# Performance work log

Measured on AMD Instinct MI355X. Metric: run time of the kernel, lower is better.

## Reference

```python
import jax, jax.numpy as jnp
import numpy as np

N_NODES = 50000
N_EDGES = 800000
IN_DIM = 256
OUT_DIM = 64
NEG_SLOPE = 0.01  # torch F.leaky_relu default


def setup_inputs() -> dict:
    key = jax.random.key(0)
    k1, k2, k3, k4, k5 = jax.random.split(key, 5)
    return {
        "h": jax.random.normal(k1, (N_NODES, IN_DIM), dtype=jnp.float32),
        "src": jax.random.randint(k2, (N_EDGES,), 0, N_NODES, dtype=jnp.int32),
        "dst": jax.random.randint(k3, (N_EDGES,), 0, N_NODES, dtype=jnp.int32),
        "W_fc": jax.random.normal(k4, (IN_DIM, OUT_DIM), dtype=jnp.float32) / np.sqrt(IN_DIM),
        "a_vec": jax.random.normal(k5, (2 * OUT_DIM,), dtype=jnp.float32) / np.sqrt(2 * OUT_DIM),
    }


def reference(h, src, dst, W_fc, a_vec):
    n = h.shape[0]
    d = W_fc.shape[1]
    # z = fc(h)
    z = h @ W_fc  # [N, out_dim]
    # edge attention: attn_fc(cat[z_src, z_dst]) == z_src@a[:d] + z_dst@a[d:]
    s_src = z @ a_vec[:d]  # [N]
    s_dst = z @ a_vec[d:]  # [N]
    e = jax.nn.leaky_relu(s_src[src] + s_dst[dst], negative_slope=NEG_SLOPE)  # [E]
    # segment softmax over incoming edges of each dst node (stable)
    e_max = jax.ops.segment_max(e, dst, num_segments=n)  # -inf for isolated nodes (unused)
    e_exp = jnp.exp(e - e_max[dst])
    denom = jax.ops.segment_sum(e_exp, dst, num_segments=n)
    alpha = e_exp / denom[dst]  # [E]
    # weighted scatter-sum of source features
    out = jax.ops.segment_sum(alpha[:, None] * z[src], dst, num_segments=n)  # [N, out_dim]
    return out
```

## Files before the change

kernel.cpp:

```cpp
#include <hip/hip_runtime.h>

#define IN_DIM 256
#define OUT_DIM 64
#define NEG_SLOPE 0.01f
#define SCAN_CHUNK 2048
#define HBS 280

typedef short short8 __attribute__((ext_vector_type(8)));
typedef float f32x4 __attribute__((ext_vector_type(4)));
typedef unsigned short u16x4 __attribute__((ext_vector_type(4)));
typedef unsigned short u16x8 __attribute__((ext_vector_type(8)));

__device__ __forceinline__ unsigned short f2b(float f) {
    unsigned u = __float_as_uint(f);
    return (unsigned short)((u + 0x7FFFu + ((u >> 16) & 1u)) >> 16);
}
__device__ __forceinline__ float b2f(unsigned short b) {
    return __uint_as_float(((unsigned)b) << 16);
}

__global__ __launch_bounds__(256) void w_conv(const float* __restrict__ W,
                                              unsigned short* __restrict__ Wt) {
    int g = blockIdx.x * 256 + threadIdx.x;
    int k = g >> 6, c = g & 63;
    Wt[c * IN_DIM + k] = f2b(W[k * OUT_DIM + c]);
}

__global__ __launch_bounds__(256) void gemm_mfma(const float* __restrict__ h,
                                                 const unsigned short* __restrict__ Wt,
                                                 const float* __restrict__ a,
                                                 unsigned short* __restrict__ zb,
                                                 float* __restrict__ s_src,
                                                 float* __restrict__ s_dst, int n) {
    __shared__ unsigned short hb[64 * HBS];
    __shared__ unsigned short wb[64 * HBS];
    __shared__ float sp1[2][64];
    __shared__ float sp2[2][64];
    const int tid = threadIdx.x;
    const int lane = tid & 63;
    const int w = tid >> 6;
    const int row0 = blockIdx.x * 64;

    {
        int c = tid >> 2, seg = tid & 3;
        #pragma unroll
        for (int i = 0; i < 8; ++i) {
            u16x8 v = *(const u16x8*)&Wt[c * IN_DIM + seg * 64 + i * 8];
            *(u16x8*)&wb[c * HBS + seg * 64 + i * 8] = v;
        }
    }
    {
        int r = tid >> 2, seg = tid & 3;
        int grow = row0 + r;
        #pragma unroll
        for (int i = 0; i < 16; ++i) {
            float4 hv = make_float4(0.f, 0.f, 0.f, 0.f);
            if (grow < n)
                hv = *(const float4*)&h[(size_t)grow * IN_DIM + seg * 64 + i * 4];
            u16x4 p;
            p[0] = f2b(hv.x); p[1] = f2b(hv.y); p[2] = f2b(hv.z); p[3] = f2b(hv.w);
            *(u16x4*)&hb[r * HBS + seg * 64 + i * 4] = p;
        }
    }
    __syncthreads();

    const int rw = (w & 1) * 32;
    const int cw = (w >> 1) * 32;
    const int l16 = lane & 15;
    const int q = lane >> 4;

    f32x4 acc[2][2] = {};
    #pragma unroll
    for (int ks = 0; ks < 8; ++ks) {
        short8 af[2], bf[2];
        #pragma unroll
        for (int i = 0; i < 2; ++i)
            af[i] = *(const short8*)&hb[(rw + i * 16 + l16) * HBS + ks * 32 + q * 8];
        #pragma unroll
        for (int j = 0; j < 2; ++j)
            bf[j] = *(const short8*)&wb[(cw + j * 16 + l16) * HBS + ks * 32 + q * 8];
        #pragma unroll
        for (int i = 0; i < 2; ++i)
            #pragma unroll
            for (int j = 0; j < 2; ++j)
                acc[i][j] = __builtin_amdgcn_mfma_f32_16x16x32_bf16(af[i], bf[j], acc[i][j], 0, 0, 0);
    }

    #pragma unroll
    for (int i = 0; i < 2; ++i) {
        #pragma unroll
        for (int reg = 0; reg < 4; ++reg) {
            int row_local = rw + i * 16 + q * 4 + reg;
            int grow = row0 + row_local;
            float p1 = 0.f, p2 = 0.f;
            #pragma unroll
            for (int j = 0; j < 2; ++j) {
                int col = cw + j * 16 + l16;
                float zv = acc[i][j][reg];
                if (grow < n) zb[(size_t)grow * OUT_DIM + col] = f2b(zv);
                p1 = fmaf(zv, a[col], p1);
                p2 = fmaf(zv, a[OUT_DIM + col], p2);
            }
            #pragma unroll
            for (int o = 1; o < 16; o <<= 1) {
                p1 += __shfl_xor(p1, o);
                p2 += __shfl_xor(p2, o);
            }
            if (l16 == 0) {
                sp1[w >> 1][row_local] = p1;
                sp2[w >> 1][row_local] = p2;
            }
        }
    }
    __syncthreads();
    if (tid < 64) {
        int grow = row0 + tid;
        if (grow < n) {
            s_src[grow] = sp1[0][tid] + sp1[1][tid];
            s_dst[grow] = sp2[0][tid] + sp2[1][tid];
        }
    }
}

__global__ __launch_bounds__(256) void count_deg(const int* __restrict__ dst,
                                                 int* __restrict__ deg,
                                                 int* __restrict__ rank, int E) {
    int i = blockIdx.x * 256 + threadIdx.x;
    if (i >= E) return;
    rank[i] = atomicAdd(&deg[dst[i]], 1);
}

__global__ __launch_bounds__(256) void block_sums(const int* __restrict__ deg,
                                                  int* __restrict__ bsum, int n) {
    __shared__ int red[256];
    const int tid = threadIdx.x;
    int base = blockIdx.x * SCAN_CHUNK + tid * 8;
    int s = 0;
    #pragma unroll
    for (int j = 0; j < 8; ++j)
        if (base + j < n) s += deg[base + j];
    red[tid] = s;
    __syncthreads();
    #pragma unroll
    for (int d = 128; d; d >>= 1) {
        if (tid < d) red[tid] += red[tid + d];
        __syncthreads();
    }
    if (tid == 0) bsum[blockIdx.x] = red[0];
}

__global__ __launch_bounds__(256) void scan_bsums(const int* __restrict__ bsum,
                                                  int* __restrict__ ebase,
                                                  int* __restrict__ off, int nb, int n) {
    __shared__ int ts[256];
    const int tid = threadIdx.x;
    int v = (tid < nb) ? bsum[tid] : 0;
    ts[tid] = v;
    __syncthreads();
    #pragma unroll
    for (int d = 1; d < 256; d <<= 1) {
        int add = (tid >= d) ? ts[tid - d] : 0;
        __syncthreads();
        ts[tid] += add;
        __syncthreads();
    }
    if (tid < nb) ebase[tid] = ts[tid] - v;
    if (tid == 255) off[n] = ts[255];
}

__global__ __launch_bounds__(256) void scan_local(const int* __restrict__ deg,
                                                  const int* __restrict__ ebase,
                                                  int* __restrict__ off, int n) {
    __shared__ int ts[256];
    const int tid = threadIdx.x;
    int base = blockIdx.x * SCAN_CHUNK + tid * 8;
    int v[8];
    int s = 0;
    #pragma unroll
    for (int j = 0; j < 8; ++j) {
        v[j] = (base + j < n) ? deg[base + j] : 0;
        s += v[j];
    }
    ts[tid] = s;
    __syncthreads();
    #pragma unroll
    for (int d = 1; d < 256; d <<= 1) {
        int add = (tid >= d) ? ts[tid - d] : 0;
        __syncthreads();
        ts[tid] += add;
        __syncthreads();
    }
    int run = ebase[blockIdx.x] + ts[tid] - s;
    #pragma unroll
    for (int j = 0; j < 8; ++j) {
        if (base + j < n) off[base + j] = run;
        run += v[j];
    }
}

__global__ __launch_bounds__(256) void scatter_csr(const int* __restrict__ src,
                                                   const int* __restrict__ dst,
                                                   const float* __restrict__ s_src,
                                                   const float* __restrict__ s_dst,
                                                   const int* __restrict__ off,
                                                   const int* __restrict__ rank,
                                                   int2* __restrict__ csr, int E) {
    int i = blockIdx.x * 256 + threadIdx.x;
    if (i >= E) return;
    int s = src[i], t = dst[i];
    float x = s_src[s] + s_dst[t];
    x = x > 0.f ? x : NEG_SLOPE * x;
    float w = __expf(x);
    int pos = off[t] + rank[i];
    csr[pos] = make_int2(s, __float_as_int(w));
}

__global__ __launch_bounds__(256) void aggregate(const int* __restrict__ off,
                                                 const int2* __restrict__ csr,
                                                 const unsigned short* __restrict__ zb,
                                                 float* __restrict__ out, int n) {
    int node = blockIdx.x * 4 + (threadIdx.x >> 6);
    int lane = threadIdx.x & 63;
    if (node >= n) return;
    int beg = off[node];
    int end = off[node + 1];

    float acc = 0.f;
    float s = 0.f;
    int j = beg;
    for (; j + 3 < end; j += 4) {
        int2 e0 = csr[j];
        int2 e1 = csr[j + 1];
        int2 e2 = csr[j + 2];
        int2 e3 = csr[j + 3];
        float w0 = __int_as_float(e0.y);
        float w1 = __int_as_float(e1.y);
        float w2 = __int_as_float(e2.y);
        float w3 = __int_as_float(e3.y);
        float z0 = b2f(zb[(size_t)e0.x * OUT_DIM + lane]);
        float z1 = b2f(zb[(size_t)e1.x * OUT_DIM + lane]);
        float z2 = b2f(zb[(size_t)e2.x * OUT_DIM + lane]);
        float z3 = b2f(zb[(size_t)e3.x * OUT_DIM + lane]);
        acc = fmaf(w0, z0, acc);
        acc = fmaf(w1, z1, acc);
        acc = fmaf(w2, z2, acc);
        acc = fmaf(w3, z3, acc);
        s += (w0 + w1) + (w2 + w3);
    }
    for (; j < end; ++j) {
        int2 e0 = csr[j];
        float w0 = __int_as_float(e0.y);
        acc = fmaf(w0, b2f(zb[(size_t)e0.x * OUT_DIM + lane]), acc);
        s += w0;
    }
    float inv = (end > beg) ? 1.0f / s : 0.f;
    out[(size_t)node * OUT_DIM + lane] = acc * inv;
}

extern "C" void kernel_launch(void* const* d_in, const int* in_sizes, int n_in,
                              void* d_out, int out_size, void* d_ws, size_t ws_size,
                              hipStream_t stream) {
    const float* h   = (const float*)d_in[0];
    const int*   src = (const int*)d_in[1];
    const int*   dst = (const int*)d_in[2];
    const float* W   = (const float*)d_in[3];
    const float* a   = (const float*)d_in[4];
    float* out = (float*)d_out;

    const int n = in_sizes[0] / IN_DIM;
    const int E = in_sizes[1];
    const int nb = (n + SCAN_CHUNK - 1) / SCAN_CHUNK;

    char* ws = (char*)d_ws;
    size_t off_b = 0;
    auto alloc = [&](size_t bytes) -> void* {
        void* p = ws + off_b;
        off_b += (bytes + 255) & ~(size_t)255;
        return p;
    };
    unsigned short* zb   = (unsigned short*)alloc((size_t)n * OUT_DIM * sizeof(unsigned short));
    unsigned short* Wt   = (unsigned short*)alloc((size_t)IN_DIM * OUT_DIM * sizeof(unsigned short));
    float*          s_src= (float*)alloc((size_t)n * sizeof(float));
    float*          s_dst= (float*)alloc((size_t)n * sizeof(float));
    int*            deg  = (int*)alloc((size_t)n * sizeof(int));
    int*            offs = (int*)alloc((size_t)(n + 1) * sizeof(int));
    int*            rank = (int*)alloc((size_t)E * sizeof(int));
    int*            bsum = (int*)alloc(256 * sizeof(int));
    int*            ebase= (int*)alloc(256 * sizeof(int));
    int2*           csr  = (int2*)alloc((size_t)E * sizeof(int2));

    hipMemsetAsync(deg, 0, (size_t)n * sizeof(int), stream);

    w_conv<<<64, 256, 0, stream>>>(W, Wt);
    gemm_mfma<<<(n + 63) / 64, 256, 0, stream>>>(h, Wt, a, zb, s_src, s_dst, n);
    count_deg<<<(E + 255) / 256, 256, 0, stream>>>(dst, deg, rank, E);
    block_sums<<<nb, 256, 0, stream>>>(deg, bsum, n);
    scan_bsums<<<1, 256, 0, stream>>>(bsum, ebase, offs, nb, n);
    scan_local<<<nb, 256, 0, stream>>>(deg, ebase, offs, n);
    scatter_csr<<<(E + 255) / 256, 256, 0, stream>>>(src, dst, s_src, s_dst, offs,
                                                     rank, csr, E);
    aggregate<<<(n + 3) / 4, 256, 0, stream>>>(offs, csr, zb, out, n);
}
```

Measured before the change: 208.6 us.

## Fuse W conversion into GEMM, merge scan passes, vectorize aggregation

Removes the separate W transpose/convert kernel by having each GEMM block load fp32 W and write bf16 transposed into shared memory. Merges the block-sum and top-level scan kernels using a last-block ticket counter. Reworks aggregation so each wavefront processes four edges concurrently with 4-wide bf16 loads, then reduces across quarter-waves with shuffles. The aim is fewer launches and more memory parallelism, at the cost of redundant W conversion in every GEMM block and strided LDS writes.

```diff
diff --git a/kernel.cpp b/kernel.cpp
--- a/kernel.cpp
+++ b/kernel.cpp
@@ -9,7 +9,6 @@
 typedef short short8 __attribute__((ext_vector_type(8)));
 typedef float f32x4 __attribute__((ext_vector_type(4)));
 typedef unsigned short u16x4 __attribute__((ext_vector_type(4)));
-typedef unsigned short u16x8 __attribute__((ext_vector_type(8)));
 
 __device__ __forceinline__ unsigned short f2b(float f) {
     unsigned u = __float_as_uint(f);
@@ -19,15 +18,8 @@
     return __uint_as_float(((unsigned)b) << 16);
 }
 
-__global__ __launch_bounds__(256) void w_conv(const float* __restrict__ W,
-                                              unsigned short* __restrict__ Wt) {
-    int g = blockIdx.x * 256 + threadIdx.x;
-    int k = g >> 6, c = g & 63;
-    Wt[c * IN_DIM + k] = f2b(W[k * OUT_DIM + c]);
-}
-
 __global__ __launch_bounds__(256) void gemm_mfma(const float* __restrict__ h,
-                                                 const unsigned short* __restrict__ Wt,
+                                                 const float* __restrict__ W,
                                                  const float* __restrict__ a,
                                                  unsigned short* __restrict__ zb,
                                                  float* __restrict__ s_src,
@@ -42,11 +34,16 @@
     const int row0 = blockIdx.x * 64;
 
     {
-        int c = tid >> 2, seg = tid & 3;
-        #pragma unroll
-        for (int i = 0; i < 8; ++i) {
-            u16x8 v = *(const u16x8*)&Wt[c * IN_DIM + seg * 64 + i * 8];
-            *(u16x8*)&wb[c * HBS + seg * 64 + i * 8] = v;
+        int c4 = (tid & 15) * 4;
+        int kb = (tid >> 4) * 16;
+        #pragma unroll
+        for (int kk = 0; kk < 16; ++kk) {
+            int k = kb + kk;
+            float4 wv = *(const float4*)&W[(size_t)k * OUT_DIM + c4];
+            wb[(c4 + 0) * HBS + k] = f2b(wv.x);
+            wb[(c4 + 1) * HBS + k] = f2b(wv.y);
+            wb[(c4 + 2) * HBS + k] = f2b(wv.z);
+            wb[(c4 + 3) * HBS + k] = f2b(wv.w);
         }
     }
     {
@@ -130,9 +127,13 @@
     rank[i] = atomicAdd(&deg[dst[i]], 1);
 }
 
-__global__ __launch_bounds__(256) void block_sums(const int* __restrict__ deg,
-                                                  int* __restrict__ bsum, int n) {
+__global__ __launch_bounds__(256) void scan_sums(const int* __restrict__ deg,
+                                                 int* __restrict__ bsum,
+                                                 int* __restrict__ ebase,
+                                                 int* __restrict__ offs,
+                                                 int* __restrict__ ticket, int n, int nb) {
     __shared__ int red[256];
+    __shared__ int lastFlag;
     const int tid = threadIdx.x;
     int base = blockIdx.x * SCAN_CHUNK + tid * 8;
     int s = 0;
@@ -146,16 +147,38 @@
         if (tid < d) red[tid] += red[tid + d];
         __syncthreads();
     }
-    if (tid == 0) bsum[blockIdx.x] = red[0];
-}
-
-__global__ __launch_bounds__(256) void scan_bsums(const int* __restrict__ bsum,
-                                                  int* __restrict__ ebase,
-                                                  int* __restrict__ off, int nb, int n) {
+    if (tid == 0) {
+        bsum[blockIdx.x] = red[0];
+        __threadfence();
+        int t = atomicAdd(ticket, 1);
+        lastFlag = (t == nb - 1);
+    }
+    __syncthreads();
+    if (lastFlag && tid == 0) {
+        int run = 0;
+        for (int b = 0; b < nb; ++b) {
+            int v = atomicAdd(&bsum[b], 0);
+            ebase[b] = run;
+            run += v;
+        }
+        offs[n] = run;
+    }
+}
+
+__global__ __launch_bounds__(256) void scan_local(const int* __restrict__ deg,
+                                                  const int* __restrict__ ebase,
+                                                  int* __restrict__ offs, int n) {
     __shared__ int ts[256];
     const int tid = threadIdx.x;
-    int v = (tid < nb) ? bsum[tid] : 0;
-    ts[tid] = v;
+    int base = blockIdx.x * SCAN_CHUNK + tid * 8;
+    int v[8];
+    int s = 0;
+    #pragma unroll
+    for (int j = 0; j < 8; ++j) {
+        v[j] = (base + j < n) ? deg[base + j] : 0;
+        s += v[j];
+    }
+    ts[tid] = s;
     __syncthreads();
     #pragma unroll
     for (int d = 1; d < 256; d <<= 1) {
@@ -164,36 +187,10 @@
         ts[tid] += add;
         __syncthreads();
     }
-    if (tid < nb) ebase[tid] = ts[tid] - v;
-    if (tid == 255) off[n] = ts[255];
-}
-
-__global__ __launch_bounds__(256) void scan_local(const int* __restrict__ deg,
-                                                  const int* __restrict__ ebase,
-                                                  int* __restrict__ off, int n) {
-    __shared__ int ts[256];
-    const int tid = threadIdx.x;
-    int base = blockIdx.x * SCAN_CHUNK + tid * 8;
-    int v[8];
-    int s = 0;
+    int run = ebase[blockIdx.x] + ts[tid] - s;
     #pragma unroll
     for (int j = 0; j < 8; ++j) {
-        v[j] = (base + j < n) ? deg[base + j] : 0;
-        s += v[j];
-    }
-    ts[tid] = s;
-    __syncthreads();
-    #pragma unroll
-    for (int d = 1; d < 256; d <<= 1) {
-        int add = (tid >= d) ? ts[tid - d] : 0;
-        __syncthreads();
-        ts[tid] += add;
-        __syncthreads();
-    }
-    int run = ebase[blockIdx.x] + ts[tid] - s;
-    #pragma unroll
-    for (int j = 0; j < 8; ++j) {
-        if (base + j < n) off[base + j] = run;
+        if (base + j < n) offs[base + j] = run;
         run += v[j];
     }
 }
@@ -202,7 +199,7 @@
                                                    const int* __restrict__ dst,
                                                    const float* __restrict__ s_src,
                                                    const float* __restrict__ s_dst,
-                                                   const int* __restrict__ off,
+                                                   const int* __restrict__ offs,
                                                    const int* __restrict__ rank,
                                                    int2* __restrict__ csr, int E) {
     int i = blockIdx.x * 256 + threadIdx.x;
@@ -211,50 +208,58 @@
     float x = s_src[s] + s_dst[t];
     x = x > 0.f ? x : NEG_SLOPE * x;
     float w = __expf(x);
-    int pos = off[t] + rank[i];
+    int pos = offs[t] + rank[i];
     csr[pos] = make_int2(s, __float_as_int(w));
 }
 
-__global__ __launch_bounds__(256) void aggregate(const int* __restrict__ off,
+__global__ __launch_bounds__(256) void aggregate(const int* __restrict__ offs,
                                                  const int2* __restrict__ csr,
                                                  const unsigned short* __restrict__ zb,
                                                  float* __restrict__ out, int n) {
     int node = blockIdx.x * 4 + (threadIdx.x >> 6);
     int lane = threadIdx.x & 63;
     if (node >= n) return;
-    int beg = off[node];
-    int end = off[node + 1];
-
-    float acc = 0.f;
+    const int q = lane >> 4;
+    const int l = lane & 15;
+    int beg = offs[node];
+    int end = offs[node + 1];
+
+    f32x4 acc = {0.f, 0.f, 0.f, 0.f};
     float s = 0.f;
-    int j = beg;
-    for (; j + 3 < end; j += 4) {
+    int j = beg + q;
+    for (; j + 4 < end; j += 8) {
         int2 e0 = csr[j];
-        int2 e1 = csr[j + 1];
-        int2 e2 = csr[j + 2];
-        int2 e3 = csr[j + 3];
+        int2 e1 = csr[j + 4];
         float w0 = __int_as_float(e0.y);
         float w1 = __int_as_float(e1.y);
-        float w2 = __int_as_float(e2.y);
-        float w3 = __int_as_float(e3.y);
-        float z0 = b2f(zb[(size_t)e0.x * OUT_DIM + lane]);
-        float z1 = b2f(zb[(size_t)e1.x * OUT_DIM + lane]);
-        float z2 = b2f(zb[(size_t)e2.x * OUT_DIM + lane]);
-        float z3 = b2f(zb[(size_t)e3.x * OUT_DIM + lane]);
-        acc = fmaf(w0, z0, acc);
-        acc = fmaf(w1, z1, acc);
-        acc = fmaf(w2, z2, acc);
-        acc = fmaf(w3, z3, acc);
-        s += (w0 + w1) + (w2 + w3);
-    }
-    for (; j < end; ++j) {
+        u16x4 z0 = *(const u16x4*)&zb[(size_t)e0.x * OUT_DIM + l * 4];
+        u16x4 z1 = *(const u16x4*)&zb[(size_t)e1.x * OUT_DIM + l * 4];
+        #pragma unroll
+        for (int k = 0; k < 4; ++k) {
+            acc[k] = fmaf(w0, b2f(z0[k]), acc[k]);
+            acc[k] = fmaf(w1, b2f(z1[k]), acc[k]);
+        }
+        s += w0 + w1;
+    }
+    for (; j < end; j += 4) {
         int2 e0 = csr[j];
         float w0 = __int_as_float(e0.y);
-        acc = fmaf(w0, b2f(zb[(size_t)e0.x * OUT_DIM + lane]), acc);
+        u16x4 z0 = *(const u16x4*)&zb[(size_t)e0.x * OUT_DIM + l * 4];
+        #pragma unroll
+        for (int k = 0; k < 4; ++k) acc[k] = fmaf(w0, b2f(z0[k]), acc[k]);
         s += w0;
     }
-    float inv = (end > beg) ? 1.0f / s : 0.f;
-    out[(size_t)node * OUT_DIM + lane] = acc * inv;
+    #pragma unroll
+    for (int o = 16; o < 64; o <<= 1) {
+        #pragma unroll
+        for (int k = 0; k < 4; ++k) acc[k] += __shfl_xor(acc[k], o);
+        s += __shfl_xor(s, o);
+    }
+    if (q == 0) {
+        float inv = (end > beg) ? 1.0f / s : 0.f;
+        float4 o = make_float4(acc[0] * inv, acc[1] * inv, acc[2] * inv, acc[3] * inv);
+        *(float4*)&out[(size_t)node * OUT_DIM + l * 4] = o;
+    }
 }
 
 extern "C" void kernel_launch(void* const* d_in, const int* in_sizes, int n_in,
@@ -278,24 +283,22 @@
         off_b += (bytes + 255) & ~(size_t)255;
         return p;
     };
-    unsigned short* zb   = (unsigned short*)alloc((size_t)n * OUT_DIM * sizeof(unsigned short));
-    unsigned short* Wt   = (unsigned short*)alloc((size_t)IN_DIM * OUT_DIM * sizeof(unsigned short));
-    float*          s_src= (float*)alloc((size_t)n * sizeof(float));
-    float*          s_dst= (float*)alloc((size_t)n * sizeof(float));
-    int*            deg  = (int*)alloc((size_t)n * sizeof(int));
-    int*            offs = (int*)alloc((size_t)(n + 1) * sizeof(int));
-    int*            rank = (int*)alloc((size_t)E * sizeof(int));
-    int*            bsum = (int*)alloc(256 * sizeof(int));
-    int*            ebase= (int*)alloc(256 * sizeof(int));
-    int2*           csr  = (int2*)alloc((size_t)E * sizeof(int2));
-
-    hipMemsetAsync(deg, 0, (size_t)n * sizeof(int), stream);
-
-    w_conv<<<64, 256, 0, stream>>>(W, Wt);
-    gemm_mfma<<<(n + 63) / 64, 256, 0, stream>>>(h, Wt, a, zb, s_src, s_dst, n);
+    unsigned short* zb    = (unsigned short*)alloc((size_t)n * OUT_DIM * sizeof(unsigned short));
+    float*          s_src = (float*)alloc((size_t)n * sizeof(float));
+    float*          s_dst = (float*)alloc((size_t)n * sizeof(float));
+    int*            deg   = (int*)alloc((size_t)(n + 64) * sizeof(int));
+    int*            ticket= deg + n;
+    int*            offs  = (int*)alloc((size_t)(n + 1) * sizeof(int));
+    int*            rank  = (int*)alloc((size_t)E * sizeof(int));
+    int*            bsum  = (int*)alloc(256 * sizeof(int));
+    int*            ebase = (int*)alloc(256 * sizeof(int));
+    int2*           csr   = (int2*)alloc((size_t)E * sizeof(int2));
+
+    hipMemsetAsync(deg, 0, (size_t)(n + 1) * sizeof(int), stream);
+
+    gemm_mfma<<<(n + 63) / 64, 256, 0, stream>>>(h, W, a, zb, s_src, s_dst, n);
     count_deg<<<(E + 255) / 256, 256, 0, stream>>>(dst, deg, rank, E);
-    block_sums<<<nb, 256, 0, stream>>>(deg, bsum, n);
-    scan_bsums<<<1, 256, 0, stream>>>(bsum, ebase, offs, nb, n);
+    scan_sums<<<nb, 256, 0, stream>>>(deg, bsum, ebase, offs, ticket, n, nb);
     scan_local<<<nb, 256, 0, stream>>>(deg, ebase, offs, n);
     scatter_csr<<<(E + 255) / 256, 256, 0, stream>>>(src, dst, s_src, s_dst, offs,
                                                      rank, csr, E);
```

Result: faster. 199.7 us (-4.3%).
